# Optimization experiments

Hardware: AMD Instinct MI355X
Metric: run time of the kernel (lower is better)

The kernel has to match this reference:

```python
import jax, jax.numpy as jnp
import numpy as np
import math

B, T, C = 4, 2048, 1024
NH = 16
HS = C // NH

def setup_inputs() -> dict:
    key = jax.random.key(0)
    ks = jax.random.split(key, 5)
    s = 0.02
    return {
        "x": jax.random.normal(ks[0], (B, T, C), dtype=jnp.float32),
        "W_attn": jax.random.normal(ks[1], (C, 3 * C), dtype=jnp.float32) * s,
        "b_attn": jax.random.normal(ks[2], (3 * C,), dtype=jnp.float32) * s,
        "W_proj": jax.random.normal(ks[3], (C, C), dtype=jnp.float32) * s,
        "b_proj": jax.random.normal(ks[4], (C,), dtype=jnp.float32) * s,
    }

def reference(x, W_attn, b_attn, W_proj, b_proj):
    Bx, Tx, Cx = x.shape
    qkv = x @ W_attn + b_attn                      # [B,T,3C]
    q, k, v = jnp.split(qkv, 3, axis=-1)
    # [B,T,C] -> [B,nh,T,hs]
    def heads(t):
        return t.reshape(Bx, Tx, NH, HS).transpose(0, 2, 1, 3)
    q, k, v = heads(q), heads(k), heads(v)
    att = jnp.einsum('bhqd,bhkd->bhqk', q, k) * (1.0 / math.sqrt(HS))
    causal = jnp.tril(jnp.ones((Tx, Tx), dtype=bool))
    att = jnp.where(causal[None, None], att, -jnp.inf)
    att = jax.nn.softmax(att, axis=-1)
    y = jnp.einsum('bhqk,bhkd->bhqd', att, v)      # [B,nh,T,hs]
    y = y.transpose(0, 2, 1, 3).reshape(Bx, Tx, Cx)
    return y @ W_proj + b_proj
```

## Files before the change

kernel.cpp:

```cpp
#include <hip/hip_runtime.h>
#include <hip/hip_bf16.h>
#include <stdint.h>

typedef __bf16 bf16x8 __attribute__((ext_vector_type(8)));
typedef __bf16 bf16x4 __attribute__((ext_vector_type(4)));
typedef float  f32x4  __attribute__((ext_vector_type(4)));

#define MFMA16(a, b, c) __builtin_amdgcn_mfma_f32_16x16x32_bf16((a), (b), (c), 0, 0, 0)

constexpr int BATCH = 4;
constexpr int TSEQ  = 2048;
constexpr int CDIM  = 1024;
constexpr int NHEAD = 16;
constexpr int HSZ   = 64;
constexpr size_t HEADELEMS = (size_t)BATCH * NHEAD * TSEQ * HSZ;

constexpr int LDF = 72;

__device__ __forceinline__ void load_lds_128(const __bf16* g, __bf16* l) {
    __builtin_amdgcn_global_load_lds(
        (const __attribute__((address_space(1))) unsigned int*)g,
        (__attribute__((address_space(3))) unsigned int*)l,
        16, 0, 0);
}

__global__ void conv_f32_bf16(const float* __restrict__ src, __bf16* __restrict__ dst, int n)
{
    const int i0 = (blockIdx.x * 256 + threadIdx.x) * 8;
    if (i0 >= n) return;
    float4 a = *(const float4*)(src + i0);
    float4 b = *(const float4*)(src + i0 + 4);
    bf16x8 o;
    o[0] = (__bf16)a.x; o[1] = (__bf16)a.y; o[2] = (__bf16)a.z; o[3] = (__bf16)a.w;
    o[4] = (__bf16)b.x; o[5] = (__bf16)b.y; o[6] = (__bf16)b.z; o[7] = (__bf16)b.w;
    *(bf16x8*)(dst + i0) = o;
}

__global__ void conv_transpose_bf16(const float* __restrict__ src, __bf16* __restrict__ dst,
                                    int K, int N)
{
    __shared__ __bf16 tile[32][33];
    const int n0 = blockIdx.x * 32, k0 = blockIdx.y * 32;
    const int tx = threadIdx.x & 31, ty = threadIdx.x >> 5;
    #pragma unroll
    for (int i = 0; i < 32; i += 8)
        tile[ty + i][tx] = (__bf16)src[(size_t)(k0 + ty + i) * N + n0 + tx];
    __syncthreads();
    #pragma unroll
    for (int i = 0; i < 32; i += 8)
        dst[(size_t)(n0 + ty + i) * K + k0 + tx] = tile[tx][ty + i];
}

template<int EPI>
__global__ __launch_bounds__(256, 4)
void gemm_bt(const __bf16* __restrict__ A, const __bf16* __restrict__ BT,
             const float* __restrict__ bias, void* __restrict__ outv,
             int M, int N, int K)
{
    __shared__ __bf16 As[2][128 * 32];
    __shared__ __bf16 Bs[2][128 * 32];

    const int t    = threadIdx.x;
    const int wave = t >> 6, lane = t & 63;
    const int quad = lane >> 4, l16 = lane & 15;
    const int bm = blockIdx.y * 128, bn = blockIdx.x * 128;
    const int wm = (wave >> 1) * 64, wn = (wave & 1) * 64;

    const int lrow = lane >> 2, lchunk = lane & 3;

    f32x4 acc[4][4];
    #pragma unroll
    for (int i = 0; i < 4; ++i)
        #pragma unroll
        for (int j = 0; j < 4; ++j)
            acc[i][j] = (f32x4){0.f, 0.f, 0.f, 0.f};

    const int c0 = wave * 2, c1 = wave * 2 + 1;
    const __bf16* a0 = A  + (size_t)(bm + 16 * c0 + lrow) * K + 8 * lchunk;
    const __bf16* a1 = A  + (size_t)(bm + 16 * c1 + lrow) * K + 8 * lchunk;
    const __bf16* b0 = BT + (size_t)(bn + 16 * c0 + lrow) * K + 8 * lchunk;
    const __bf16* b1 = BT + (size_t)(bn + 16 * c1 + lrow) * K + 8 * lchunk;

    const int nk = K >> 5;
    load_lds_128(a0, &As[0][c0 * 512]);
    load_lds_128(a1, &As[0][c1 * 512]);
    load_lds_128(b0, &Bs[0][c0 * 512]);
    load_lds_128(b1, &Bs[0][c1 * 512]);

    for (int it = 0; it < nk; ++it) {
        asm volatile("s_waitcnt vmcnt(0)" ::: "memory");
        __syncthreads();
        const int cur = it & 1, nxt = cur ^ 1;
        if (it + 1 < nk) {
            const int k0 = (it + 1) * 32;
            load_lds_128(a0 + k0, &As[nxt][c0 * 512]);
            load_lds_128(a1 + k0, &As[nxt][c1 * 512]);
            load_lds_128(b0 + k0, &Bs[nxt][c0 * 512]);
            load_lds_128(b1 + k0, &Bs[nxt][c1 * 512]);
        }

        bf16x8 af[4], bfr[4];
        #pragma unroll
        for (int i = 0; i < 4; ++i)
            af[i]  = *(const bf16x8*)(&As[cur][(wm + i * 16 + l16) * 32 + quad * 8]);
        #pragma unroll
        for (int i = 0; i < 4; ++i)
            bfr[i] = *(const bf16x8*)(&Bs[cur][(wn + i * 16 + l16) * 32 + quad * 8]);
        #pragma unroll
        for (int mi = 0; mi < 4; ++mi)
            #pragma unroll
            for (int ni = 0; ni < 4; ++ni)
                acc[mi][ni] = MFMA16(af[mi], bfr[ni], acc[mi][ni]);
    }

    if constexpr (EPI == 0) {
        __bf16* outp = (__bf16*)outv;
        #pragma unroll
        for (int ni = 0; ni < 4; ++ni) {
            const int col = bn + wn + ni * 16 + l16;
            const float bv = bias[col];
            const int which = col >> 10;
            const int c = col & 1023;
            const int h = c >> 6, d = c & 63;
            #pragma unroll
            for (int mi = 0; mi < 4; ++mi)
                #pragma unroll
                for (int r = 0; r < 4; ++r) {
                    const int row = bm + wm + mi * 16 + quad * 4 + r;
                    const int bb = row >> 11, tt = row & 2047;
                    size_t idx;
                    if (which == 2)
                        idx = 2 * HEADELEMS + ((((size_t)bb * NHEAD + h) * HSZ + d) * TSEQ + tt);
                    else
                        idx = (size_t)which * HEADELEMS
                            + ((((size_t)bb * NHEAD + h) * TSEQ + tt) * HSZ + d);
                    outp[idx] = (__bf16)(acc[mi][ni][r] + bv);
                }
        }
    } else {
        float* outp = (float*)outv;
        #pragma unroll
        for (int ni = 0; ni < 4; ++ni) {
            const int col = bn + wn + ni * 16 + l16;
            const float bv = bias[col];
            #pragma unroll
            for (int mi = 0; mi < 4; ++mi)
                #pragma unroll
                for (int r = 0; r < 4; ++r) {
                    const int row = bm + wm + mi * 16 + quad * 4 + r;
                    outp[(size_t)row * N + col] = acc[mi][ni][r] + bv;
                }
        }
    }
}

__global__ __launch_bounds__(256, 4)
void flash_attn(const __bf16* __restrict__ Q, const __bf16* __restrict__ Kg,
                const __bf16* __restrict__ Vg, __bf16* __restrict__ Y)
{
    __shared__ __bf16 Ks[64 * LDF];
    __shared__ __bf16 Vs[64 * LDF];
    __shared__ __bf16 Ps[4][32 * LDF];

    const int t = threadIdx.x, wave = t >> 6, lane = t & 63;
    const int quad = lane >> 4, l16 = lane & 15;
    const int bh = blockIdx.x;
    const int q0 = ((int)gridDim.y - 1 - (int)blockIdx.y) * 128;
    const size_t base = (size_t)bh * TSEQ * HSZ;

    const float sc = 0.125f * 1.44269504088896341f;

    bf16x8 qf[2][2];
    #pragma unroll
    for (int mi = 0; mi < 2; ++mi) {
        const int qrow = q0 + wave * 32 + mi * 16 + l16;
        #pragma unroll
        for (int h = 0; h < 2; ++h) {
            bf16x8 raw = *(const bf16x8*)(Q + base + (size_t)qrow * HSZ + h * 32 + quad * 8);
            #pragma unroll
            for (int j = 0; j < 8; ++j) qf[mi][h][j] = (__bf16)((float)raw[j] * sc);
        }
    }

    bf16x8 ones;
    #pragma unroll
    for (int j = 0; j < 8; ++j) ones[j] = (__bf16)1.0f;

    f32x4 oacc[2][4];
    f32x4 lacc[2];
    #pragma unroll
    for (int mi = 0; mi < 2; ++mi) {
        lacc[mi] = (f32x4){0.f, 0.f, 0.f, 0.f};
        #pragma unroll
        for (int dt = 0; dt < 4; ++dt) oacc[mi][dt] = (f32x4){0.f, 0.f, 0.f, 0.f};
    }

    const int s_row = t >> 2, s_c16 = (t & 3) * 16;

    const int iters = q0 / 64 + 2;
    for (int it = 0; it < iters; ++it) {
        const int kt = it * 64;
        {
            const __bf16* kp = Kg + base + (size_t)(kt + s_row) * HSZ + s_c16;
            bf16x8 v0 = *(const bf16x8*)kp;
            bf16x8 v1 = *(const bf16x8*)(kp + 8);
            *(bf16x8*)(&Ks[s_row * LDF + s_c16])     = v0;
            *(bf16x8*)(&Ks[s_row * LDF + s_c16 + 8]) = v1;
        }
        {
            const __bf16* vp = Vg + base + (size_t)s_row * TSEQ + kt + s_c16;
            bf16x8 v0 = *(const bf16x8*)vp;
            bf16x8 v1 = *(const bf16x8*)(vp + 8);
            *(bf16x8*)(&Vs[s_row * LDF + s_c16])     = v0;
            *(bf16x8*)(&Vs[s_row * LDF + s_c16 + 8]) = v1;
        }
        __syncthreads();

        const bool active = (kt <= q0 + wave * 32 + 31);
        if (active) {
            f32x4 st[4][2];
            #pragma unroll
            for (int ktl = 0; ktl < 4; ++ktl) {
                bf16x8 kf0 = *(const bf16x8*)(&Ks[(ktl * 16 + l16) * LDF + quad * 8]);
                bf16x8 kf1 = *(const bf16x8*)(&Ks[(ktl * 16 + l16) * LDF + 32 + quad * 8]);
                #pragma unroll
                for (int mi = 0; mi < 2; ++mi) {
                    f32x4 a = (f32x4){0.f, 0.f, 0.f, 0.f};
                    a = MFMA16(kf0, qf[mi][0], a);
                    a = MFMA16(kf1, qf[mi][1], a);
                    st[ktl][mi] = a;
                }
            }

            if (kt + 63 >= q0 + wave * 32) {
                #pragma unroll
                for (int ktl = 0; ktl < 4; ++ktl)
                    #pragma unroll
                    for (int mi = 0; mi < 2; ++mi)
                        #pragma unroll
                        for (int r = 0; r < 4; ++r) {
                            const int key = kt + ktl * 16 + quad * 4 + r;
                            const int qr  = q0 + wave * 32 + mi * 16 + l16;
                            if (key > qr) st[ktl][mi][r] = -1e30f;
                        }
            }

            #pragma unroll
            for (int ktl = 0; ktl < 4; ++ktl)
                #pragma unroll
                for (int mi = 0; mi < 2; ++mi) {
                    bf16x4 pv;
                    #pragma unroll
                    for (int r = 0; r < 4; ++r)
                        pv[r] = (__bf16)exp2f(st[ktl][mi][r]);
                    *(bf16x4*)(&Ps[wave][(mi * 16 + l16) * LDF + ktl * 16 + quad * 4]) = pv;
                }

            asm volatile("s_waitcnt lgkmcnt(0)" ::: "memory");

            bf16x8 pf[2][2];
            #pragma unroll
            for (int mi = 0; mi < 2; ++mi) {
                pf[mi][0] = *(const bf16x8*)(&Ps[wave][(mi * 16 + l16) * LDF + quad * 8]);
                pf[mi][1] = *(const bf16x8*)(&Ps[wave][(mi * 16 + l16) * LDF + 32 + quad * 8]);
                lacc[mi] = MFMA16(pf[mi][0], ones, lacc[mi]);
                lacc[mi] = MFMA16(pf[mi][1], ones, lacc[mi]);
            }
            #pragma unroll
            for (int dt = 0; dt < 4; ++dt) {
                bf16x8 vf0 = *(const bf16x8*)(&Vs[(dt * 16 + l16) * LDF + quad * 8]);
                bf16x8 vf1 = *(const bf16x8*)(&Vs[(dt * 16 + l16) * LDF + 32 + quad * 8]);
                #pragma unroll
                for (int mi = 0; mi < 2; ++mi) {
                    oacc[mi][dt] = MFMA16(pf[mi][0], vf0, oacc[mi][dt]);
                    oacc[mi][dt] = MFMA16(pf[mi][1], vf1, oacc[mi][dt]);
                }
            }
        }
        __syncthreads();
    }

    const int b = bh >> 4, h = bh & 15;
    #pragma unroll
    for (int mi = 0; mi < 2; ++mi) {
        const f32x4 linv = {1.f / lacc[mi][0], 1.f / lacc[mi][1],
                            1.f / lacc[mi][2], 1.f / lacc[mi][3]};
        #pragma unroll
        for (int dt = 0; dt < 4; ++dt)
            #pragma unroll
            for (int r = 0; r < 4; ++r) {
                const int tt = q0 + wave * 32 + mi * 16 + quad * 4 + r;
                const int d  = dt * 16 + l16;
                Y[((size_t)(b * TSEQ + tt) * CDIM) + h * HSZ + d] =
                    (__bf16)(oacc[mi][dt][r] * linv[r]);
            }
    }
}

extern "C" void kernel_launch(void* const* d_in, const int* in_sizes, int n_in,
                              void* d_out, int out_size, void* d_ws, size_t ws_size,
                              hipStream_t stream)
{
    const int NX = 8388608, NWA = 3145728, NWP = 1048576;
    char* wsb = (char*)d_ws;

    size_t off = 0;
    __bf16* cx   = (__bf16*)(wsb + off); off += (size_t)2 * NX;
    __bf16* cwaT = (__bf16*)(wsb + off); off += (size_t)2 * NWA;
    __bf16* cwpT = (__bf16*)(wsb + off); off += (size_t)2 * NWP;
    __bf16* q    = (__bf16*)(wsb + off);
    __bf16* y    = q + 3 * HEADELEMS;

    const float* xf = (const float*)d_in[0];
    const float* ba = (const float*)d_in[2];
    const float* bp = (const float*)d_in[4];

    conv_f32_bf16<<<NX / 2048, 256, 0, stream>>>(xf, cx, NX);
    conv_transpose_bf16<<<dim3(3 * CDIM / 32, CDIM / 32), 256, 0, stream>>>(
        (const float*)d_in[1], cwaT, CDIM, 3 * CDIM);
    conv_transpose_bf16<<<dim3(CDIM / 32, CDIM / 32), 256, 0, stream>>>(
        (const float*)d_in[3], cwpT, CDIM, CDIM);

    gemm_bt<0><<<dim3(3 * CDIM / 128, BATCH * TSEQ / 128), 256, 0, stream>>>(
        cx, cwaT, ba, q, BATCH * TSEQ, 3 * CDIM, CDIM);

    flash_attn<<<dim3(BATCH * NHEAD, TSEQ / 128), 256, 0, stream>>>(
        q, q + HEADELEMS, q + 2 * HEADELEMS, y);

    gemm_bt<1><<<dim3(CDIM / 128, BATCH * TSEQ / 128), 256, 0, stream>>>(
        y, cwpT, bp, d_out, BATCH * TSEQ, CDIM, CDIM);
}
```

Measured before the change: 271.4 us.

## Add 256x256-tile QKV GEMM with XCD-aware block remapping and interleaved prefetch

```diff
diff --git a/kernel.cpp b/kernel.cpp
--- a/kernel.cpp
+++ b/kernel.cpp
@@ -49,6 +49,168 @@
     #pragma unroll
     for (int i = 0; i < 32; i += 8)
         dst[(size_t)(n0 + ty + i) * K + k0 + tx] = tile[tx][ty + i];
+}
+
+__global__ __launch_bounds__(512, 2)
+void gemm_qkv_256(const __bf16* __restrict__ A, const __bf16* __restrict__ BT,
+                  const float* __restrict__ bias, __bf16* __restrict__ outp,
+                  int M, int N, int K)
+{
+    __shared__ __bf16 As[2][2][256 * 32];
+    __shared__ __bf16 Bs[2][2][256 * 32];
+
+    const int t    = threadIdx.x;
+    const int wave = t >> 6, lane = t & 63;
+    const int quad = lane >> 4, l16 = lane & 15;
+    const int wm = (wave >> 2) * 128, wn = (wave & 3) * 64;
+
+    const int nbx = (int)gridDim.x;
+    const int nwg = nbx * (int)gridDim.y;
+    int lin = (int)blockIdx.y * nbx + (int)blockIdx.x;
+    {
+        const int q8 = nwg >> 3, r8 = nwg & 7;
+        const int xcd = lin & 7, idx = lin >> 3;
+        lin = (xcd < r8 ? xcd * (q8 + 1) : r8 * (q8 + 1) + (xcd - r8) * q8) + idx;
+    }
+    const int bm = (lin / nbx) * 256, bn = (lin % nbx) * 256;
+
+    const int srow = wave * 16 + (lane >> 2);
+    const int scol = (lane & 3) * 8;
+    const __bf16* gA0 = A  + (size_t)(bm + srow) * K + scol;
+    const __bf16* gA1 = A  + (size_t)(bm + 128 + srow) * K + scol;
+    const __bf16* gB0 = BT + (size_t)(bn + srow) * K + scol;
+    const __bf16* gB1 = BT + (size_t)(bn + 128 + srow) * K + scol;
+    const int dst0 = wave * 512;
+    const int dst1 = 4096 + wave * 512;
+
+    const int aoff = (wm + l16) * 32 + quad * 8;
+    const int boff = (wn + l16) * 32 + quad * 8;
+
+    f32x4 acc[8][4];
+    #pragma unroll
+    for (int i = 0; i < 8; ++i)
+        #pragma unroll
+        for (int j = 0; j < 4; ++j)
+            acc[i][j] = (f32x4){0.f, 0.f, 0.f, 0.f};
+
+    const int nt = K >> 6;
+
+#define STAGE_A(buf, slab, kofs) do { \
+    load_lds_128(gA0 + (kofs) + (slab) * 32, &As[buf][slab][dst0]); \
+    load_lds_128(gA1 + (kofs) + (slab) * 32, &As[buf][slab][dst1]); } while (0)
+#define STAGE_B(buf, slab, kofs) do { \
+    load_lds_128(gB0 + (kofs) + (slab) * 32, &Bs[buf][slab][dst0]); \
+    load_lds_128(gB1 + (kofs) + (slab) * 32, &Bs[buf][slab][dst1]); } while (0)
+
+    STAGE_A(0, 0, 0); STAGE_B(0, 0, 0);
+    STAGE_A(0, 1, 0); STAGE_B(0, 1, 0);
+    asm volatile("s_waitcnt vmcnt(4)" ::: "memory");
+    __builtin_amdgcn_s_barrier();
+
+    for (int it = 0; it < nt; ++it) {
+        const int cur = it & 1, nxt = cur ^ 1;
+        const int k1 = (it + 1) << 6;
+        const bool pf = (it + 1 < nt);
+        const __bf16* As0 = &As[cur][0][0];
+        const __bf16* As1 = &As[cur][1][0];
+        const __bf16* Bs0 = &Bs[cur][0][0];
+        const __bf16* Bs1 = &Bs[cur][1][0];
+
+        bf16x8 af[4], bfr[4];
+
+        #pragma unroll
+        for (int ni = 0; ni < 4; ++ni) bfr[ni] = *(const bf16x8*)(Bs0 + boff + ni * 512);
+        #pragma unroll
+        for (int mi = 0; mi < 4; ++mi) af[mi] = *(const bf16x8*)(As0 + aoff + mi * 512);
+        if (pf) STAGE_A(nxt, 0, k1);
+        __builtin_amdgcn_s_barrier();
+        asm volatile("s_waitcnt lgkmcnt(0)" ::: "memory");
+        __builtin_amdgcn_sched_barrier(0);
+        __builtin_amdgcn_s_setprio(1);
+        #pragma unroll
+        for (int mi = 0; mi < 4; ++mi)
+            #pragma unroll
+            for (int ni = 0; ni < 4; ++ni)
+                acc[mi][ni] = MFMA16(af[mi], bfr[ni], acc[mi][ni]);
+        __builtin_amdgcn_s_setprio(0);
+        __builtin_amdgcn_s_barrier();
+
+        #pragma unroll
+        for (int mi = 0; mi < 4; ++mi) af[mi] = *(const bf16x8*)(As0 + aoff + (mi + 4) * 512);
+        if (pf) STAGE_B(nxt, 0, k1);
+        __builtin_amdgcn_s_barrier();
+        asm volatile("s_waitcnt lgkmcnt(0)" ::: "memory");
+        __builtin_amdgcn_sched_barrier(0);
+        __builtin_amdgcn_s_setprio(1);
+        #pragma unroll
+        for (int mi = 0; mi < 4; ++mi)
+            #pragma unroll
+            for (int ni = 0; ni < 4; ++ni)
+                acc[mi + 4][ni] = MFMA16(af[mi], bfr[ni], acc[mi + 4][ni]);
+        __builtin_amdgcn_s_setprio(0);
+        if (pf) asm volatile("s_waitcnt vmcnt(4)" ::: "memory");
+        else    asm volatile("s_waitcnt vmcnt(0)" ::: "memory");
+        __builtin_amdgcn_s_barrier();
+
+        #pragma unroll
+        for (int ni = 0; ni < 4; ++ni) bfr[ni] = *(const bf16x8*)(Bs1 + boff + ni * 512);
+        #pragma unroll
+        for (int mi = 0; mi < 4; ++mi) af[mi] = *(const bf16x8*)(As1 + aoff + mi * 512);
+        if (pf) STAGE_A(nxt, 1, k1);
+        __builtin_amdgcn_s_barrier();
+        asm volatile("s_waitcnt lgkmcnt(0)" ::: "memory");
+        __builtin_amdgcn_sched_barrier(0);
+        __builtin_amdgcn_s_setprio(1);
+        #pragma unroll
+        for (int mi = 0; mi < 4; ++mi)
+            #pragma unroll
+            for (int ni = 0; ni < 4; ++ni)
+                acc[mi][ni] = MFMA16(af[mi], bfr[ni], acc[mi][ni]);
+        __builtin_amdgcn_s_setprio(0);
+        __builtin_amdgcn_s_barrier();
+
+        #pragma unroll
+        for (int mi = 0; mi < 4; ++mi) af[mi] = *(const bf16x8*)(As1 + aoff + (mi + 4) * 512);
+        if (pf) STAGE_B(nxt, 1, k1);
+        __builtin_amdgcn_s_barrier();
+        asm volatile("s_waitcnt lgkmcnt(0)" ::: "memory");
+        __builtin_amdgcn_sched_barrier(0);
+        __builtin_amdgcn_s_setprio(1);
+        #pragma unroll
+        for (int mi = 0; mi < 4; ++mi)
+            #pragma unroll
+            for (int ni = 0; ni < 4; ++ni)
+                acc[mi + 4][ni] = MFMA16(af[mi], bfr[ni], acc[mi + 4][ni]);
+        __builtin_amdgcn_s_setprio(0);
+        if (pf) asm volatile("s_waitcnt vmcnt(4)" ::: "memory");
+        else    asm volatile("s_waitcnt vmcnt(0)" ::: "memory");
+        __builtin_amdgcn_s_barrier();
+    }
+#undef STAGE_A
+#undef STAGE_B
+
+    #pragma unroll
+    for (int ni = 0; ni < 4; ++ni) {
+        const int col = bn + wn + ni * 16 + l16;
+        const float bv = bias[col];
+        const int which = col >> 10;
+        const int c = col & 1023;
+        const int h = c >> 6, d = c & 63;
+        #pragma unroll
+        for (int mi = 0; mi < 8; ++mi)
+            #pragma unroll
+            for (int r = 0; r < 4; ++r) {
+                const int row = bm + wm + mi * 16 + quad * 4 + r;
+                const int bb = row >> 11, tt = row & 2047;
+                size_t idx;
+                if (which == 2)
+                    idx = 2 * HEADELEMS + ((((size_t)bb * NHEAD + h) * HSZ + d) * TSEQ + tt);
+                else
+                    idx = (size_t)which * HEADELEMS
+                        + ((((size_t)bb * NHEAD + h) * TSEQ + tt) * HSZ + d);
+                outp[idx] = (__bf16)(acc[mi][ni][r] + bv);
+            }
+    }
 }
 
 template<int EPI>
@@ -321,7 +483,7 @@
     conv_transpose_bf16<<<dim3(CDIM / 32, CDIM / 32), 256, 0, stream>>>(
         (const float*)d_in[3], cwpT, CDIM, CDIM);
 
-    gemm_bt<0><<<dim3(3 * CDIM / 128, BATCH * TSEQ / 128), 256, 0, stream>>>(
+    gemm_qkv_256<<<dim3(3 * CDIM / 256, BATCH * TSEQ / 256), 512, 0, stream>>>(
         cx, cwaT, ba, q, BATCH * TSEQ, 3 * CDIM, CDIM);
 
     flash_attn<<<dim3(BATCH * NHEAD, TSEQ / 128), 256, 0, stream>>>(
```

New measurement: 284.2 us. 4.7% more time.

## Prefetch next K/V tile into registers in attention; use 64-row proj GEMM tiles

Applied to the files above, without the earlier changes.

```diff
diff --git a/kernel.cpp b/kernel.cpp
--- a/kernel.cpp
+++ b/kernel.cpp
@@ -155,6 +155,78 @@
 }
 
 __global__ __launch_bounds__(256, 4)
+void gemm_bt64(const __bf16* __restrict__ A, const __bf16* __restrict__ BT,
+               const float* __restrict__ bias, float* __restrict__ outp,
+               int M, int N, int K)
+{
+    __shared__ __bf16 As[2][64 * 32];
+    __shared__ __bf16 Bs[2][128 * 32];
+
+    const int t    = threadIdx.x;
+    const int wave = t >> 6, lane = t & 63;
+    const int quad = lane >> 4, l16 = lane & 15;
+    const int bm = blockIdx.y * 64, bn = blockIdx.x * 128;
+    const int wm = (wave >> 1) * 32, wn = (wave & 1) * 64;
+
+    const int lrow = lane >> 2, lchunk = lane & 3;
+
+    f32x4 acc[2][4];
+    #pragma unroll
+    for (int i = 0; i < 2; ++i)
+        #pragma unroll
+        for (int j = 0; j < 4; ++j)
+            acc[i][j] = (f32x4){0.f, 0.f, 0.f, 0.f};
+
+    const int c0 = wave * 2, c1 = wave * 2 + 1;
+    const __bf16* a0 = A  + (size_t)(bm + 16 * wave + lrow) * K + 8 * lchunk;
+    const __bf16* b0 = BT + (size_t)(bn + 16 * c0 + lrow) * K + 8 * lchunk;
+    const __bf16* b1 = BT + (size_t)(bn + 16 * c1 + lrow) * K + 8 * lchunk;
+
+    const int nk = K >> 5;
+    load_lds_128(a0, &As[0][wave * 512]);
+    load_lds_128(b0, &Bs[0][c0 * 512]);
+    load_lds_128(b1, &Bs[0][c1 * 512]);
+
+    for (int it = 0; it < nk; ++it) {
+        asm volatile("s_waitcnt vmcnt(0)" ::: "memory");
+        __syncthreads();
+        const int cur = it & 1, nxt = cur ^ 1;
+        if (it + 1 < nk) {
+            const int k0 = (it + 1) * 32;
+            load_lds_128(a0 + k0, &As[nxt][wave * 512]);
+            load_lds_128(b0 + k0, &Bs[nxt][c0 * 512]);
+            load_lds_128(b1 + k0, &Bs[nxt][c1 * 512]);
+        }
+
+        bf16x8 af[2], bfr[4];
+        #pragma unroll
+        for (int i = 0; i < 2; ++i)
+            af[i]  = *(const bf16x8*)(&As[cur][(wm + i * 16 + l16) * 32 + quad * 8]);
+        #pragma unroll
+        for (int i = 0; i < 4; ++i)
+            bfr[i] = *(const bf16x8*)(&Bs[cur][(wn + i * 16 + l16) * 32 + quad * 8]);
+        #pragma unroll
+        for (int mi = 0; mi < 2; ++mi)
+            #pragma unroll
+            for (int ni = 0; ni < 4; ++ni)
+                acc[mi][ni] = MFMA16(af[mi], bfr[ni], acc[mi][ni]);
+    }
+
+    #pragma unroll
+    for (int ni = 0; ni < 4; ++ni) {
+        const int col = bn + wn + ni * 16 + l16;
+        const float bv = bias[col];
+        #pragma unroll
+        for (int mi = 0; mi < 2; ++mi)
+            #pragma unroll
+            for (int r = 0; r < 4; ++r) {
+                const int row = bm + wm + mi * 16 + quad * 4 + r;
+                outp[(size_t)row * N + col] = acc[mi][ni][r] + bv;
+            }
+    }
+}
+
+__global__ __launch_bounds__(256, 4)
 void flash_attn(const __bf16* __restrict__ Q, const __bf16* __restrict__ Kg,
                 const __bf16* __restrict__ Vg, __bf16* __restrict__ Y)
 {
@@ -196,25 +268,30 @@
     }
 
     const int s_row = t >> 2, s_c16 = (t & 3) * 16;
+    const __bf16* kbase = Kg + base + (size_t)s_row * HSZ + s_c16;
+    const __bf16* vbase = Vg + base + (size_t)s_row * TSEQ + s_c16;
+
+    bf16x8 kr0 = *(const bf16x8*)(kbase);
+    bf16x8 kr1 = *(const bf16x8*)(kbase + 8);
+    bf16x8 vr0 = *(const bf16x8*)(vbase);
+    bf16x8 vr1 = *(const bf16x8*)(vbase + 8);
 
     const int iters = q0 / 64 + 2;
     for (int it = 0; it < iters; ++it) {
         const int kt = it * 64;
-        {
-            const __bf16* kp = Kg + base + (size_t)(kt + s_row) * HSZ + s_c16;
-            bf16x8 v0 = *(const bf16x8*)kp;
-            bf16x8 v1 = *(const bf16x8*)(kp + 8);
-            *(bf16x8*)(&Ks[s_row * LDF + s_c16])     = v0;
-            *(bf16x8*)(&Ks[s_row * LDF + s_c16 + 8]) = v1;
-        }
-        {
-            const __bf16* vp = Vg + base + (size_t)s_row * TSEQ + kt + s_c16;
-            bf16x8 v0 = *(const bf16x8*)vp;
-            bf16x8 v1 = *(const bf16x8*)(vp + 8);
-            *(bf16x8*)(&Vs[s_row * LDF + s_c16])     = v0;
-            *(bf16x8*)(&Vs[s_row * LDF + s_c16 + 8]) = v1;
-        }
+        *(bf16x8*)(&Ks[s_row * LDF + s_c16])     = kr0;
+        *(bf16x8*)(&Ks[s_row * LDF + s_c16 + 8]) = kr1;
+        *(bf16x8*)(&Vs[s_row * LDF + s_c16])     = vr0;
+        *(bf16x8*)(&Vs[s_row * LDF + s_c16 + 8]) = vr1;
         __syncthreads();
+
+        if (it + 1 < iters) {
+            const int kn = kt + 64;
+            kr0 = *(const bf16x8*)(kbase + (size_t)kn * HSZ);
+            kr1 = *(const bf16x8*)(kbase + (size_t)kn * HSZ + 8);
+            vr0 = *(const bf16x8*)(vbase + kn);
+            vr1 = *(const bf16x8*)(vbase + kn + 8);
+        }
 
         const bool active = (kt <= q0 + wave * 32 + 31);
         if (active) {
@@ -327,6 +404,6 @@
     flash_attn<<<dim3(BATCH * NHEAD, TSEQ / 128), 256, 0, stream>>>(
         q, q + HEADELEMS, q + 2 * HEADELEMS, y);
 
-    gemm_bt<1><<<dim3(CDIM / 128, BATCH * TSEQ / 128), 256, 0, stream>>>(
-        y, cwpT, bp, d_out, BATCH * TSEQ, CDIM, CDIM);
-}
+    gemm_bt64<<<dim3(CDIM / 128, BATCH * TSEQ / 64), 256, 0, stream>>>(
+        y, cwpT, bp, (float*)d_out, BATCH * TSEQ, CDIM, CDIM);
+}
```

Result: slower. 296.1 us (+9.1%).

## Prefetch next K/V tile into registers in flash attention; split QKV GEMM launch

Applied to the files above, without the earlier changes.

```diff
diff --git a/kernel.cpp b/kernel.cpp
--- a/kernel.cpp
+++ b/kernel.cpp
@@ -55,7 +55,7 @@
 __global__ __launch_bounds__(256, 4)
 void gemm_bt(const __bf16* __restrict__ A, const __bf16* __restrict__ BT,
              const float* __restrict__ bias, void* __restrict__ outv,
-             int M, int N, int K)
+             int M, int N, int K, int rowoff)
 {
     __shared__ __bf16 As[2][128 * 32];
     __shared__ __bf16 Bs[2][128 * 32];
@@ -126,7 +126,7 @@
             for (int mi = 0; mi < 4; ++mi)
                 #pragma unroll
                 for (int r = 0; r < 4; ++r) {
-                    const int row = bm + wm + mi * 16 + quad * 4 + r;
+                    const int row = rowoff + bm + wm + mi * 16 + quad * 4 + r;
                     const int bb = row >> 11, tt = row & 2047;
                     size_t idx;
                     if (which == 2)
@@ -147,7 +147,7 @@
             for (int mi = 0; mi < 4; ++mi)
                 #pragma unroll
                 for (int r = 0; r < 4; ++r) {
-                    const int row = bm + wm + mi * 16 + quad * 4 + r;
+                    const int row = rowoff + bm + wm + mi * 16 + quad * 4 + r;
                     outp[(size_t)row * N + col] = acc[mi][ni][r] + bv;
                 }
         }
@@ -196,25 +196,30 @@
     }
 
     const int s_row = t >> 2, s_c16 = (t & 3) * 16;
+    const __bf16* kbase = Kg + base + (size_t)s_row * HSZ + s_c16;
+    const __bf16* vbase = Vg + base + (size_t)s_row * TSEQ + s_c16;
+
+    bf16x8 kr0 = *(const bf16x8*)(kbase);
+    bf16x8 kr1 = *(const bf16x8*)(kbase + 8);
+    bf16x8 vr0 = *(const bf16x8*)(vbase);
+    bf16x8 vr1 = *(const bf16x8*)(vbase + 8);
 
     const int iters = q0 / 64 + 2;
     for (int it = 0; it < iters; ++it) {
         const int kt = it * 64;
-        {
-            const __bf16* kp = Kg + base + (size_t)(kt + s_row) * HSZ + s_c16;
-            bf16x8 v0 = *(const bf16x8*)kp;
-            bf16x8 v1 = *(const bf16x8*)(kp + 8);
-            *(bf16x8*)(&Ks[s_row * LDF + s_c16])     = v0;
-            *(bf16x8*)(&Ks[s_row * LDF + s_c16 + 8]) = v1;
-        }
-        {
-            const __bf16* vp = Vg + base + (size_t)s_row * TSEQ + kt + s_c16;
-            bf16x8 v0 = *(const bf16x8*)vp;
-            bf16x8 v1 = *(const bf16x8*)(vp + 8);
-            *(bf16x8*)(&Vs[s_row * LDF + s_c16])     = v0;
-            *(bf16x8*)(&Vs[s_row * LDF + s_c16 + 8]) = v1;
-        }
+        *(bf16x8*)(&Ks[s_row * LDF + s_c16])     = kr0;
+        *(bf16x8*)(&Ks[s_row * LDF + s_c16 + 8]) = kr1;
+        *(bf16x8*)(&Vs[s_row * LDF + s_c16])     = vr0;
+        *(bf16x8*)(&Vs[s_row * LDF + s_c16 + 8]) = vr1;
         __syncthreads();
+
+        if (it + 1 < iters) {
+            const int kn = kt + 64;
+            kr0 = *(const bf16x8*)(kbase + (size_t)kn * HSZ);
+            kr1 = *(const bf16x8*)(kbase + (size_t)kn * HSZ + 8);
+            vr0 = *(const bf16x8*)(vbase + kn);
+            vr1 = *(const bf16x8*)(vbase + kn + 8);
+        }
 
         const bool active = (kt <= q0 + wave * 32 + 31);
         if (active) {
@@ -321,12 +326,14 @@
     conv_transpose_bf16<<<dim3(CDIM / 32, CDIM / 32), 256, 0, stream>>>(
         (const float*)d_in[3], cwpT, CDIM, CDIM);
 
-    gemm_bt<0><<<dim3(3 * CDIM / 128, BATCH * TSEQ / 128), 256, 0, stream>>>(
-        cx, cwaT, ba, q, BATCH * TSEQ, 3 * CDIM, CDIM);
+    gemm_bt<0><<<dim3(3 * CDIM / 128, 32), 256, 0, stream>>>(
+        cx, cwaT, ba, q, BATCH * TSEQ / 2, 3 * CDIM, CDIM, 0);
+    gemm_bt<0><<<dim3(3 * CDIM / 128, 32), 256, 0, stream>>>(
+        cx + (size_t)4096 * CDIM, cwaT, ba, q, BATCH * TSEQ / 2, 3 * CDIM, CDIM, 4096);
 
     flash_attn<<<dim3(BATCH * NHEAD, TSEQ / 128), 256, 0, stream>>>(
         q, q + HEADELEMS, q + 2 * HEADELEMS, y);
 
     gemm_bt<1><<<dim3(CDIM / 128, BATCH * TSEQ / 128), 256, 0, stream>>>(
-        y, cwpT, bp, d_out, BATCH * TSEQ, CDIM, CDIM);
-}
+        y, cwpT, bp, d_out, BATCH * TSEQ, CDIM, CDIM, 0);
+}
```

Measured after the change: 285.9 us. 1.05x slower.
